# Kernel tuning notes

Hardware: AMD Instinct MI355X
Metric: run time of the kernel (lower is better)

## Reference

```python
import jax, jax.numpy as jnp
import numpy as np

N, R, IN_DIM, OUT_DIM, MODE = 16, 128, 64, 64, 16


def setup_inputs() -> dict:
    key = jax.random.key(0)
    k1, k2, k3, k4, k5 = jax.random.split(key, 5)
    # xavier_normal-like scale used by the torch init:
    # std = gain * sqrt(2/(fan_in+fan_out)) with gain = sqrt(in+out)/(in*out)
    fan = IN_DIM * OUT_DIM * MODE * MODE  # torch fans over last-dim slices; scale is tiny either way
    w_std = (1.0 / (IN_DIM * OUT_DIM)) * np.sqrt(IN_DIM + OUT_DIM)
    return {
        "X": jax.random.normal(k1, (N, R, R, IN_DIM), dtype=jnp.float32),
        "w_res": jax.random.normal(k2, (IN_DIM, OUT_DIM), dtype=jnp.float32) / np.sqrt(IN_DIM),
        "b_res": jax.random.normal(k3, (OUT_DIM,), dtype=jnp.float32) * 0.01,
        "fw0": jax.random.normal(k4, (IN_DIM, OUT_DIM, MODE, MODE, 2), dtype=jnp.float32) * w_std,
        "fw1": jax.random.normal(k5, (IN_DIM, OUT_DIM, MODE, MODE, 2), dtype=jnp.float32) * w_std,
    }


def reference(X, w_res, b_res, fw0, fw1):
    # X: [N, r, r, in_dim]
    n, r, _, _ = X.shape
    m = MODE
    res = X @ w_res + b_res                          # [N, r, r, out]
    Xp = jnp.transpose(X, (0, 3, 1, 2))              # [N, in, r, r]
    X_ft = jnp.fft.rfft2(Xp, s=(r, r), norm="ortho")  # [N, in, r, r//2+1] complex
    W0 = fw0[..., 0] + 1j * fw0[..., 1]              # [in, out, m, m] complex
    W1 = fw1[..., 0] + 1j * fw1[..., 1]
    top = jnp.einsum("nihw,iohw->nohw", X_ft[:, :, :m, :m], W0)
    bot = jnp.einsum("nihw,iohw->nohw", X_ft[:, :, -m:, :m], W1)
    Out_ft = jnp.zeros((n, OUT_DIM, r, r // 2 + 1), dtype=top.dtype)
    Out_ft = Out_ft.at[:, :, :m, :m].set(top)
    Out_ft = Out_ft.at[:, :, -m:, :m].set(bot)
    Y = jnp.fft.irfft2(Out_ft, s=(r, r), norm="ortho")  # [N, out, r, r]
    Y = jnp.transpose(Y, (0, 2, 3, 1))                   # [N, r, r, out]
    return jax.nn.silu(Y + res)
```

## Files before the change

### kernel.cpp

```cpp
#include <hip/hip_runtime.h>

#define NBATCH 16
#define RSZ 128
#define ICH 64
#define OCH 64
#define MODES 16
#define TMODES 32
#define PI2F 6.283185307179586f

typedef float f32x4 __attribute__((ext_vector_type(4)));
typedef short bf16x8 __attribute__((ext_vector_type(8)));

static __device__ __forceinline__ ushort f2bf(float f) {
  union { float f; unsigned u; } v;
  v.f = f;
  unsigned r = v.u + 0x7FFFu + ((v.u >> 16) & 1u);
  return (ushort)(r >> 16);
}
static __device__ __forceinline__ float b2f(ushort u) {
  union { unsigned u; float f; } v;
  v.u = ((unsigned)u) << 16;
  return v.f;
}

#define TAB_EF 4096
#define TAB_WR 8192
#define TAB_T1 12288
#define TAB_E2 28672

#define DFTX_BLOCKS 1024

__global__ __launch_bounds__(256) void k_main(const float* __restrict__ X,
                                              const float* __restrict__ fw0,
                                              const float* __restrict__ fw1,
                                              const float* __restrict__ w_res,
                                              ushort* __restrict__ Are,
                                              ushort* __restrict__ Aim,
                                              ushort* __restrict__ fwT,
                                              ushort* __restrict__ tabs) {
  const int tid = threadIdx.x;
  if (blockIdx.x >= DFTX_BLOCKS) {
    const int b = blockIdx.x - DFTX_BLOCKS;
    if (b < 128) {
      const int tensor = b >> 6, i = b & 63;
      const float* fw = tensor ? fw1 : fw0;
      const int o = tid & 63, q = tid >> 6;
      const float* src = fw + ((size_t)(i * 64 + o) * 256 + q * 64) * 2;
      ushort2* dst = (ushort2*)fwT;
#pragma unroll 4
      for (int r2 = 0; r2 < 32; ++r2) {
        float4 v = *(const float4*)(src + r2 * 4);
        int r = r2 * 2;
        int mh0 = q * 4 + (r >> 4), w0 = r & 15;
        int mh1 = q * 4 + ((r + 1) >> 4), w1 = (r + 1) & 15;
        int t0 = tensor * 16 + mh0, t1 = tensor * 16 + mh1;
        ushort2 p0, p1;
        p0.x = f2bf(v.x); p0.y = f2bf(v.y);
        p1.x = f2bf(v.z); p1.y = f2bf(v.w);
        dst[(((size_t)w0 * 32 + t0) * 64 + i) * 64 + o] = p0;
        dst[(((size_t)w1 * 32 + t1) * 64 + i) * 64 + o] = p1;
      }
      return;
    }
    __shared__ float2 ut[128];
    if (tid < 128) {
      float s, c;
      sincosf(PI2F * (float)tid * (1.0f / 128.0f), &s, &c);
      ut[tid] = make_float2(c, s);
    }
    __syncthreads();
    const int pb = b - 128;
    if (pb == 0) {
      for (int e = tid; e < 4096; e += 256) {
        int x = e >> 5, mm = e & 31, w = mm >> 1, c = mm & 1;
        float2 u = ut[(w * x) & 127];
        tabs[TAB_EF + e] = f2bf(c ? -u.y : u.x);
      }
    } else if (pb == 1) {
      for (int e = tid; e < 4096; e += 256) {
        int o = e >> 6, i = e & 63;
        tabs[TAB_WR + e] = f2bf(w_res[i * 64 + o]);
      }
    } else if (pb < 6) {
      for (int k = tid; k < 4096; k += 256) {
        int e = (pb - 2) * 4096 + k;
        int m = e >> 8, kk = e & 255;
        int y = kk & 127, pl = kk >> 7;
        int t = m & 31, imr = m >> 5;
        int h = (t < 16) ? t : (t + 96);
        float2 u = ut[(h * y) & 127];
        float val = (!imr) ? (pl ? u.y : u.x) : (pl ? u.x : -u.y);
        tabs[TAB_T1 + e] = f2bf(val);
      }
    } else {
      for (int k = tid; k < 4096; k += 256) {
        int e = (pb - 6) * 4096 + k;
        int m = e >> 6, kk = e & 63;
        int y = m & 127, imr = m >> 7;
        int t = kk & 31, pl = kk >> 5;
        int h = (t < 16) ? t : (t + 96);
        float2 u = ut[(h * y) & 127];
        float val = (!imr) ? (pl ? -u.y : u.x) : (pl ? u.x : u.y);
        tabs[TAB_E2 + e] = f2bf(val);
      }
    }
    return;
  }
  __shared__ ushort Tm[32][136];
  __shared__ ushort XT[2][64][136];
  const int row0 = blockIdx.x * 2;
  {
    int w = tid >> 4, xseg = (tid & 15) * 8;
    for (int e = 0; e < 8; ++e) {
      int x = xseg + e;
      int p = (w * x) & 127;
      float s, c;
      sincosf(PI2F * (float)p * (1.0f / 128.0f), &s, &c);
      Tm[2 * w][x] = f2bf(c);
      Tm[2 * w + 1][x] = f2bf(-s);
    }
  }
#pragma unroll
  for (int j = 0; j < 4; ++j) {
    int tt = tid + 256 * j;
    int rr = tt >> 9, r = tt & 511;
    int i0 = (r & 15) * 4, x0 = (r >> 4) * 4;
    const float* Xr = X + (size_t)(row0 + rr) * RSZ * ICH;
    float4 r0 = *(const float4*)&Xr[(x0 + 0) * ICH + i0];
    float4 r1 = *(const float4*)&Xr[(x0 + 1) * ICH + i0];
    float4 r2 = *(const float4*)&Xr[(x0 + 2) * ICH + i0];
    float4 r3 = *(const float4*)&Xr[(x0 + 3) * ICH + i0];
#pragma unroll
    for (int p = 0; p < 4; ++p) {
      int i = i0 + p;
      int col = x0 ^ ((((i) >> 2) & 7) << 3);
      ushort4 pk;
      pk.x = f2bf(((const float*)&r0)[p]);
      pk.y = f2bf(((const float*)&r1)[p]);
      pk.z = f2bf(((const float*)&r2)[p]);
      pk.w = f2bf(((const float*)&r3)[p]);
      *(ushort4*)&XT[rr][i][col] = pk;
    }
  }
  __syncthreads();
  const int wid = tid >> 6, lane = tid & 63;
  const int lr = lane & 15, lk = lane >> 4;
  const int rr = wid >> 1, nh = wid & 1;
  f32x4 acc[2][2];
#pragma unroll
  for (int mt = 0; mt < 2; ++mt)
#pragma unroll
    for (int ntl = 0; ntl < 2; ++ntl) acc[mt][ntl] = (f32x4)(0.f);
#pragma unroll
  for (int kt = 0; kt < 4; ++kt) {
    int kb = kt * 32 + lk * 8;
    bf16x8 a0 = *(const bf16x8*)&Tm[lr][kb];
    bf16x8 a1 = *(const bf16x8*)&Tm[16 + lr][kb];
    bf16x8 b[2];
#pragma unroll
    for (int ntl = 0; ntl < 2; ++ntl) {
      int i = (nh * 2 + ntl) * 16 + lr;
      int col = kb ^ (((i >> 2) & 7) << 3);
      b[ntl] = *(const bf16x8*)&XT[rr][i][col];
    }
#pragma unroll
    for (int ntl = 0; ntl < 2; ++ntl) {
      acc[0][ntl] = __builtin_amdgcn_mfma_f32_16x16x32_bf16(a0, b[ntl], acc[0][ntl], 0, 0, 0);
      acc[1][ntl] = __builtin_amdgcn_mfma_f32_16x16x32_bf16(a1, b[ntl], acc[1][ntl], 0, 0, 0);
    }
  }
  const int row = row0 + rr;
#pragma unroll
  for (int mt = 0; mt < 2; ++mt)
#pragma unroll
    for (int q = 0; q < 4; ++q) {
      int m = mt * 16 + lk * 4 + q;
      int w = m >> 1, c = m & 1;
      ushort* plane = c ? Aim : Are;
#pragma unroll
      for (int ntl = 0; ntl < 2; ++ntl) {
        int i = (nh * 2 + ntl) * 16 + lr;
        plane[((size_t)row * MODES + w) * ICH + i] = f2bf(acc[mt][ntl][q]);
      }
    }
}

__global__ __launch_bounds__(512) void k_mid(const ushort* __restrict__ Are,
                                             const ushort* __restrict__ Aim,
                                             const ushort* __restrict__ tabs,
                                             const ushort* __restrict__ fwT,
                                             ushort* __restrict__ D) {
  const int n = blockIdx.x >> 4;
  const int w = blockIdx.x & 15;
  __shared__ ushort As[64][264];
  __shared__ float2 Bls[32][66];
  __shared__ ushort Cs[64][72];
  const int tid = threadIdx.x;
#pragma unroll
  for (int e = 0; e < 2; ++e) {
    int tt = e * 512 + tid;
    int pl = tt >> 9, r = tt & 511;
    int i0 = (r & 15) * 4, y0 = (r >> 4) * 4;
    const ushort* P = pl ? Aim : Are;
    const ushort* base = P + (((size_t)(n * RSZ + y0) * MODES + w) * ICH + i0);
    ushort4 r0 = *(const ushort4*)(base + 0 * MODES * ICH);
    ushort4 r1 = *(const ushort4*)(base + 1 * MODES * ICH);
    ushort4 r2 = *(const ushort4*)(base + 2 * MODES * ICH);
    ushort4 r3 = *(const ushort4*)(base + 3 * MODES * ICH);
    const ushort* q0 = (const ushort*)&r0;
    const ushort* q1 = (const ushort*)&r1;
    const ushort* q2 = (const ushort*)&r2;
    const ushort* q3 = (const ushort*)&r3;
#pragma unroll
    for (int p = 0; p < 4; ++p) {
      ushort4 pk;
      pk.x = q0[p]; pk.y = q1[p]; pk.z = q2[p]; pk.w = q3[p];
      *(ushort4*)&As[i0 + p][pl * 128 + y0] = pk;
    }
  }
  __syncthreads();
  const int wid = tid >> 6, lane = tid & 63;
  const int lr = lane & 15, lk = lane >> 4;
  {
    const int mt = wid >> 1, nh = wid & 1;
    f32x4 acc[2];
    acc[0] = (f32x4)(0.f);
    acc[1] = (f32x4)(0.f);
#pragma unroll
    for (int kt = 0; kt < 8; ++kt) {
      int kb = kt * 32 + lk * 8;
      bf16x8 a = *(const bf16x8*)&tabs[TAB_T1 + (mt * 16 + lr) * 256 + kb];
      bf16x8 b0 = *(const bf16x8*)&As[(nh * 2 + 0) * 16 + lr][kb];
      bf16x8 b1 = *(const bf16x8*)&As[(nh * 2 + 1) * 16 + lr][kb];
      acc[0] = __builtin_amdgcn_mfma_f32_16x16x32_bf16(a, b0, acc[0], 0, 0, 0);
      acc[1] = __builtin_amdgcn_mfma_f32_16x16x32_bf16(a, b1, acc[1], 0, 0, 0);
    }
#pragma unroll
    for (int nt2 = 0; nt2 < 2; ++nt2)
#pragma unroll
      for (int q = 0; q < 4; ++q) {
        int m = mt * 16 + lk * 4 + q;
        int t = m & 31, pl = m >> 5;
        int i = (nh * 2 + nt2) * 16 + lr;
        ((float*)&Bls[t][i])[pl] = acc[nt2][q];
      }
  }
  __syncthreads();
  const float sc = (w == 0) ? (1.f / 16384.f) : (2.f / 16384.f);
  float2 cacc[4];
  const ushort2* fwT2 = (const ushort2*)fwT;
#pragma unroll
  for (int p = 0; p < 4; ++p) {
    const int t = p * 8 + wid;
    const ushort2* Wcol = fwT2 + (size_t)(w * 32 + t) * 4096 + lane;
    float cr = 0.f, ci = 0.f;
#pragma unroll 8
    for (int i = 0; i < 64; ++i) {
      ushort2 wv = Wcol[i * 64];
      float wr = b2f(wv.x), wi = b2f(wv.y);
      float2 b = Bls[t][i];
      cr += b.x * wr - b.y * wi;
      ci += b.x * wi + b.y * wr;
    }
    cacc[p] = make_float2(cr * sc, ci * sc);
  }
  __syncthreads();
#pragma unroll
  for (int p = 0; p < 4; ++p) {
    const int t = p * 8 + wid;
    Cs[lane][t] = f2bf(cacc[p].x);
    Cs[lane][t + 32] = f2bf(cacc[p].y);
  }
  __syncthreads();
  f32x4 acc[2][4];
#pragma unroll
  for (int mi = 0; mi < 2; ++mi)
#pragma unroll
    for (int nt = 0; nt < 4; ++nt) acc[mi][nt] = (f32x4)(0.f);
#pragma unroll
  for (int kt = 0; kt < 2; ++kt) {
    int kb = kt * 32 + lk * 8;
    bf16x8 b[4];
#pragma unroll
    for (int nt = 0; nt < 4; ++nt) b[nt] = *(const bf16x8*)&Cs[nt * 16 + lr][kb];
#pragma unroll
    for (int mi = 0; mi < 2; ++mi) {
      bf16x8 a = *(const bf16x8*)&tabs[TAB_E2 + ((wid * 2 + mi) * 16 + lr) * 64 + kb];
#pragma unroll
      for (int nt = 0; nt < 4; ++nt)
        acc[mi][nt] = __builtin_amdgcn_mfma_f32_16x16x32_bf16(a, b[nt], acc[mi][nt], 0, 0, 0);
    }
  }
#pragma unroll
  for (int mi = 0; mi < 2; ++mi)
#pragma unroll
    for (int nt = 0; nt < 4; ++nt)
#pragma unroll
      for (int q = 0; q < 4; ++q) {
        int m = (wid * 2 + mi) * 16 + lk * 4 + q;
        int y = m & 127, pl = m >> 7;
        int o = nt * 16 + lr;
        D[((size_t)(n * RSZ + y) * MODES + w) * 128 + o * 2 + pl] = f2bf(acc[mi][nt][q]);
      }
}

__global__ __launch_bounds__(256) void k_final(const float* __restrict__ X,
                                               const ushort* __restrict__ D,
                                               const ushort* __restrict__ tabs,
                                               const float* __restrict__ b_res,
                                               float* __restrict__ out) {
  __shared__ ushort Ac[128][104];
  __shared__ ushort Bc[64][104];
  __shared__ float br[64];
  const int tid = threadIdx.x;
  const int row = blockIdx.x;
  const float* Xr = X + (size_t)row * RSZ * ICH;
#pragma unroll
  for (int j = 0; j < 8; ++j) {
    int k = tid + j * 256;
    int x = k >> 4, i0 = (k & 15) * 4;
    float4 v = *(const float4*)&Xr[x * ICH + i0];
    ushort4 pk;
    pk.x = f2bf(v.x); pk.y = f2bf(v.y); pk.z = f2bf(v.z); pk.w = f2bf(v.w);
    *(ushort4*)&Ac[x][i0] = pk;
  }
  {
    int x = tid >> 1, half = tid & 1;
    *(bf16x8*)&Ac[x][64 + half * 16] = *(const bf16x8*)&tabs[TAB_EF + x * 32 + half * 16];
    *(bf16x8*)&Ac[x][64 + half * 16 + 8] = *(const bf16x8*)&tabs[TAB_EF + x * 32 + half * 16 + 8];
  }
  {
    int o = tid >> 2, s = (tid & 3) * 16;
    *(bf16x8*)&Bc[o][s] = *(const bf16x8*)&tabs[TAB_WR + o * 64 + s];
    *(bf16x8*)&Bc[o][s + 8] = *(const bf16x8*)&tabs[TAB_WR + o * 64 + s + 8];
  }
#pragma unroll
  for (int j = 0; j < 4; ++j) {
    int idx = tid + j * 256;
    int w2 = idx >> 6, o = idx & 63;
    ushort2 v = *(const ushort2*)&D[(size_t)row * 2048 + w2 * 128 + o * 2];
    *(ushort2*)&Bc[o][64 + 2 * w2] = v;
  }
  if (tid < 64) br[tid] = b_res[tid];
  __syncthreads();
  const int wid = tid >> 6, lane = tid & 63;
  const int lr = lane & 15, lk = lane >> 4;
  f32x4 acc[2][4];
#pragma unroll
  for (int mi = 0; mi < 2; ++mi)
#pragma unroll
    for (int nt = 0; nt < 4; ++nt) acc[mi][nt] = (f32x4)(0.f);
#pragma unroll
  for (int kt = 0; kt < 3; ++kt) {
    int kb = kt * 32 + lk * 8;
    bf16x8 a0 = *(const bf16x8*)&Ac[(wid * 2 + 0) * 16 + lr][kb];
    bf16x8 a1 = *(const bf16x8*)&Ac[(wid * 2 + 1) * 16 + lr][kb];
    bf16x8 b[4];
#pragma unroll
    for (int nt = 0; nt < 4; ++nt) b[nt] = *(const bf16x8*)&Bc[nt * 16 + lr][kb];
#pragma unroll
    for (int nt = 0; nt < 4; ++nt) {
      acc[0][nt] = __builtin_amdgcn_mfma_f32_16x16x32_bf16(a0, b[nt], acc[0][nt], 0, 0, 0);
      acc[1][nt] = __builtin_amdgcn_mfma_f32_16x16x32_bf16(a1, b[nt], acc[1][nt], 0, 0, 0);
    }
  }
  float* orow = out + (size_t)row * RSZ * OCH;
#pragma unroll
  for (int mi = 0; mi < 2; ++mi)
#pragma unroll
    for (int nt = 0; nt < 4; ++nt)
#pragma unroll
      for (int q = 0; q < 4; ++q) {
        int x = (wid * 2 + mi) * 16 + lk * 4 + q;
        int o = nt * 16 + lr;
        float v = acc[mi][nt][q] + br[o];
        orow[x * OCH + o] = v / (1.f + __expf(-v));
      }
}

extern "C" void kernel_launch(void* const* d_in, const int* in_sizes, int n_in,
                              void* d_out, int out_size, void* d_ws, size_t ws_size,
                              hipStream_t stream) {
  (void)in_sizes; (void)n_in; (void)out_size; (void)ws_size;
  const float* X = (const float*)d_in[0];
  const float* w_res = (const float*)d_in[1];
  const float* b_res = (const float*)d_in[2];
  const float* fw0 = (const float*)d_in[3];
  const float* fw1 = (const float*)d_in[4];
  float* out = (float*)d_out;
  ushort* wsu = (ushort*)d_ws;
  ushort* Are = wsu;
  ushort* Aim = Are + 2097152;
  ushort* Dbf = Aim + 2097152;
  ushort* fwT = Dbf + 4194304;
  ushort* tabs = fwT + 4194304;
  k_main<<<DFTX_BLOCKS + 138, 256, 0, stream>>>(X, fw0, fw1, w_res, Are, Aim, fwT, tabs);
  k_mid<<<NBATCH * MODES, 512, 0, stream>>>(Are, Aim, tabs, fwT, Dbf);
  k_final<<<NBATCH * RSZ, 256, 0, stream>>>(X, Dbf, tabs, b_res, out);
}
```

Before: 69.08 us.

## Process one row per block in DFT-x stage and build twiddles from LDS table

The first-stage DFT kernel now gives each block one image row instead of two, doubling the number of blocks to 2048, with each wave computing one 16-channel tile. Per-element sincosf for the twiddle matrix is replaced by a 128-entry shared unit-root table, and global X loads are issued into registers before the table setup so memory latency overlaps it. This aims at better occupancy and latency hiding on a memory-bound stage, at the cost of recomputing the twiddle matrix in twice as many blocks.

```diff
diff --git a/kernel.cpp b/kernel.cpp
--- a/kernel.cpp
+++ b/kernel.cpp
@@ -28,7 +28,7 @@
 #define TAB_T1 12288
 #define TAB_E2 28672
 
-#define DFTX_BLOCKS 1024
+#define DFTX_BLOCKS 2048
 
 __global__ __launch_bounds__(256) void k_main(const float* __restrict__ X,
                                               const float* __restrict__ fw0,
@@ -62,18 +62,18 @@
       }
       return;
     }
-    __shared__ float2 ut[128];
+    __shared__ float2 utp[128];
     if (tid < 128) {
       float s, c;
       sincosf(PI2F * (float)tid * (1.0f / 128.0f), &s, &c);
-      ut[tid] = make_float2(c, s);
+      utp[tid] = make_float2(c, s);
     }
     __syncthreads();
     const int pb = b - 128;
     if (pb == 0) {
       for (int e = tid; e < 4096; e += 256) {
         int x = e >> 5, mm = e & 31, w = mm >> 1, c = mm & 1;
-        float2 u = ut[(w * x) & 127];
+        float2 u = utp[(w * x) & 127];
         tabs[TAB_EF + e] = f2bf(c ? -u.y : u.x);
       }
     } else if (pb == 1) {
@@ -88,7 +88,7 @@
         int y = kk & 127, pl = kk >> 7;
         int t = m & 31, imr = m >> 5;
         int h = (t < 16) ? t : (t + 96);
-        float2 u = ut[(h * y) & 127];
+        float2 u = utp[(h * y) & 127];
         float val = (!imr) ? (pl ? u.y : u.x) : (pl ? u.x : -u.y);
         tabs[TAB_T1 + e] = f2bf(val);
       }
@@ -99,77 +99,76 @@
         int y = m & 127, imr = m >> 7;
         int t = kk & 31, pl = kk >> 5;
         int h = (t < 16) ? t : (t + 96);
-        float2 u = ut[(h * y) & 127];
+        float2 u = utp[(h * y) & 127];
         float val = (!imr) ? (pl ? -u.y : u.x) : (pl ? u.x : u.y);
         tabs[TAB_E2 + e] = f2bf(val);
       }
     }
     return;
   }
+  __shared__ float2 ut[128];
   __shared__ ushort Tm[32][136];
-  __shared__ ushort XT[2][64][136];
-  const int row0 = blockIdx.x * 2;
-  {
-    int w = tid >> 4, xseg = (tid & 15) * 8;
-    for (int e = 0; e < 8; ++e) {
-      int x = xseg + e;
-      int p = (w * x) & 127;
-      float s, c;
-      sincosf(PI2F * (float)p * (1.0f / 128.0f), &s, &c);
-      Tm[2 * w][x] = f2bf(c);
-      Tm[2 * w + 1][x] = f2bf(-s);
-    }
-  }
-#pragma unroll
-  for (int j = 0; j < 4; ++j) {
-    int tt = tid + 256 * j;
-    int rr = tt >> 9, r = tt & 511;
+  __shared__ ushort XT[64][136];
+  const int row = blockIdx.x;
+  const float* Xr = X + (size_t)row * RSZ * ICH;
+  float4 rv[8];
+#pragma unroll
+  for (int e = 0; e < 2; ++e) {
+    int r = tid + e * 256;
     int i0 = (r & 15) * 4, x0 = (r >> 4) * 4;
-    const float* Xr = X + (size_t)(row0 + rr) * RSZ * ICH;
-    float4 r0 = *(const float4*)&Xr[(x0 + 0) * ICH + i0];
-    float4 r1 = *(const float4*)&Xr[(x0 + 1) * ICH + i0];
-    float4 r2 = *(const float4*)&Xr[(x0 + 2) * ICH + i0];
-    float4 r3 = *(const float4*)&Xr[(x0 + 3) * ICH + i0];
+    rv[e * 4 + 0] = *(const float4*)&Xr[(x0 + 0) * ICH + i0];
+    rv[e * 4 + 1] = *(const float4*)&Xr[(x0 + 1) * ICH + i0];
+    rv[e * 4 + 2] = *(const float4*)&Xr[(x0 + 2) * ICH + i0];
+    rv[e * 4 + 3] = *(const float4*)&Xr[(x0 + 3) * ICH + i0];
+  }
+  if (tid < 128) {
+    float s, c;
+    sincosf(PI2F * (float)tid * (1.0f / 128.0f), &s, &c);
+    ut[tid] = make_float2(c, s);
+  }
+  __syncthreads();
+#pragma unroll
+  for (int e = 0; e < 16; ++e) {
+    int idx = tid + e * 256;
+    int m = idx >> 7, x = idx & 127;
+    int w = m >> 1, c = m & 1;
+    float2 u = ut[(w * x) & 127];
+    Tm[m][x] = f2bf(c ? -u.y : u.x);
+  }
+#pragma unroll
+  for (int e = 0; e < 2; ++e) {
+    int r = tid + e * 256;
+    int i0 = (r & 15) * 4, x0 = (r >> 4) * 4;
 #pragma unroll
     for (int p = 0; p < 4; ++p) {
       int i = i0 + p;
       int col = x0 ^ ((((i) >> 2) & 7) << 3);
       ushort4 pk;
-      pk.x = f2bf(((const float*)&r0)[p]);
-      pk.y = f2bf(((const float*)&r1)[p]);
-      pk.z = f2bf(((const float*)&r2)[p]);
-      pk.w = f2bf(((const float*)&r3)[p]);
-      *(ushort4*)&XT[rr][i][col] = pk;
+      pk.x = f2bf(((const float*)&rv[e * 4 + 0])[p]);
+      pk.y = f2bf(((const float*)&rv[e * 4 + 1])[p]);
+      pk.z = f2bf(((const float*)&rv[e * 4 + 2])[p]);
+      pk.w = f2bf(((const float*)&rv[e * 4 + 3])[p]);
+      *(ushort4*)&XT[i][col] = pk;
     }
   }
   __syncthreads();
   const int wid = tid >> 6, lane = tid & 63;
   const int lr = lane & 15, lk = lane >> 4;
-  const int rr = wid >> 1, nh = wid & 1;
-  f32x4 acc[2][2];
-#pragma unroll
-  for (int mt = 0; mt < 2; ++mt)
-#pragma unroll
-    for (int ntl = 0; ntl < 2; ++ntl) acc[mt][ntl] = (f32x4)(0.f);
+  const int nt = wid;
+  f32x4 acc[2];
+  acc[0] = (f32x4)(0.f);
+  acc[1] = (f32x4)(0.f);
 #pragma unroll
   for (int kt = 0; kt < 4; ++kt) {
     int kb = kt * 32 + lk * 8;
     bf16x8 a0 = *(const bf16x8*)&Tm[lr][kb];
     bf16x8 a1 = *(const bf16x8*)&Tm[16 + lr][kb];
-    bf16x8 b[2];
-#pragma unroll
-    for (int ntl = 0; ntl < 2; ++ntl) {
-      int i = (nh * 2 + ntl) * 16 + lr;
-      int col = kb ^ (((i >> 2) & 7) << 3);
-      b[ntl] = *(const bf16x8*)&XT[rr][i][col];
-    }
-#pragma unroll
-    for (int ntl = 0; ntl < 2; ++ntl) {
-      acc[0][ntl] = __builtin_amdgcn_mfma_f32_16x16x32_bf16(a0, b[ntl], acc[0][ntl], 0, 0, 0);
-      acc[1][ntl] = __builtin_amdgcn_mfma_f32_16x16x32_bf16(a1, b[ntl], acc[1][ntl], 0, 0, 0);
-    }
-  }
-  const int row = row0 + rr;
+    int i = nt * 16 + lr;
+    int col = kb ^ (((i >> 2) & 7) << 3);
+    bf16x8 b = *(const bf16x8*)&XT[i][col];
+    acc[0] = __builtin_amdgcn_mfma_f32_16x16x32_bf16(a0, b, acc[0], 0, 0, 0);
+    acc[1] = __builtin_amdgcn_mfma_f32_16x16x32_bf16(a1, b, acc[1], 0, 0, 0);
+  }
 #pragma unroll
   for (int mt = 0; mt < 2; ++mt)
 #pragma unroll
@@ -177,11 +176,8 @@
       int m = mt * 16 + lk * 4 + q;
       int w = m >> 1, c = m & 1;
       ushort* plane = c ? Aim : Are;
-#pragma unroll
-      for (int ntl = 0; ntl < 2; ++ntl) {
-        int i = (nh * 2 + ntl) * 16 + lr;
-        plane[((size_t)row * MODES + w) * ICH + i] = f2bf(acc[mt][ntl][q]);
-      }
+      int i = nt * 16 + lr;
+      plane[((size_t)row * MODES + w) * ICH + i] = f2bf(acc[mt][q]);
     }
 }
 
```

New measurement: 67.03 us. 1.03x faster.
